# Kernel optimization log

Hardware: AMD Instinct MI355X
Metric: run time of the kernel (lower is better)

## Reference

```python
import jax, jax.numpy as jnp
import numpy as np

B, N, F_IN, K, NUM_CLASSES = 16, 2048, 8, 35, 4
EPS = 1e-5


def _bn(x, g, b):
    # BatchNorm in training mode: stats over all leading (batch/node/edge) dims.
    ax = tuple(range(x.ndim - 1))
    mu = jnp.mean(x, axis=ax, keepdims=True)
    var = jnp.var(x, axis=ax, keepdims=True)
    return g * (x - mu) * jax.lax.rsqrt(var + EPS) + b


def _edge_feats(h, k):
    # h: [B,N,C]. Dynamic kNN within each graph (self included, as torch_cluster.knn),
    # then EdgeConv features cat([x_i, x_j - x_i]) -> [B,N,k,2C].
    sq = jnp.sum(h * h, -1)                                   # [B,N]
    d = sq[:, :, None] + sq[:, None, :] - 2.0 * jnp.einsum('bnc,bmc->bnm', h, h)
    _, idx = jax.lax.top_k(-d, k)                             # [B,N,k]
    hj = jax.vmap(lambda hb, ib: hb[ib])(h, idx)              # [B,N,k,C]
    hi = jnp.broadcast_to(h[:, :, None, :], hj.shape)
    return jnp.concatenate([hi, hj - hi], axis=-1)


def _forward(x, w1, b1, g1, bt1, w2, b2, g2, bt2, w3, b3, w4, b4,
             w5, b5, w6, b6, g6, bt6, w7, b7, g7, bt7, w8, b8):
    # conv1: DynamicEdgeConv(MLP([16,64,64,64]), k, 'max'); plain_last => 3rd linear bare
    e = _edge_feats(x, K)                                     # [B,N,K,16]
    h = jax.nn.relu(_bn(e @ w1 + b1, g1, bt1))
    h = jax.nn.relu(_bn(h @ w2 + b2, g2, bt2))
    h = h @ w3 + b3
    x1 = jnp.max(h, axis=2)                                   # [B,N,64] scatter-max over k
    # conv2: DynamicEdgeConv(MLP([128,128]), k, 'max'); single plain linear
    e2 = _edge_feats(x1, K)                                   # [B,N,K,128]
    x2 = jnp.max(e2 @ w4 + b4, axis=2)                        # [B,N,128]
    out = jnp.concatenate([x1, x2], axis=-1) @ w5 + b5        # [B,N,256]
    pooled = jnp.max(out, axis=1)                             # [B,256] global_max_pool
    # head MLP([256,128,64,4], dropout eval-mode, batch_norm), plain_last
    h = jax.nn.relu(_bn(pooled @ w6 + b6, g6, bt6))
    h = jax.nn.relu(_bn(h @ w7 + b7, g7, bt7))
    return h @ w8 + b8                                        # [B,4]


def setup_inputs() -> dict:
    key = jax.random.key(0)
    ks = jax.random.split(key, 12)

    def lin(kk, fi, fo):
        k1, k2 = jax.random.split(kk)
        w = jax.random.normal(k1, (fi, fo), jnp.float32) / np.sqrt(fi).astype(np.float32)
        b = jax.random.normal(k2, (fo,), jnp.float32) * 0.01
        return w, b

    x = jax.random.normal(ks[0], (B, N, F_IN), jnp.float32)
    w1, b1 = lin(ks[1], 2 * F_IN, 64)
    w2, b2 = lin(ks[2], 64, 64)
    w3, b3 = lin(ks[3], 64, 64)
    w4, b4 = lin(ks[4], 2 * 64, 128)
    w5, b5 = lin(ks[5], 128 + 64, 256)
    w6, b6 = lin(ks[6], 256, 128)
    w7, b7 = lin(ks[7], 128, 64)
    w8, b8 = lin(ks[8], 64, NUM_CLASSES)
    ones, zeros = jnp.ones, jnp.zeros
    return {
        'x': x,
        'w1': w1, 'b1': b1, 'g1': ones(64), 'bt1': zeros(64),
        'w2': w2, 'b2': b2, 'g2': ones(64), 'bt2': zeros(64),
        'w3': w3, 'b3': b3,
        'w4': w4, 'b4': b4,
        'w5': w5, 'b5': b5,
        'w6': w6, 'b6': b6, 'g6': ones(128), 'bt6': zeros(128),
        'w7': w7, 'b7': b7, 'g7': ones(64), 'bt7': zeros(64),
        'w8': w8, 'b8': b8,
    }


def reference(x, w1, b1, g1, bt1, w2, b2, g2, bt2, w3, b3, w4, b4,
              w5, b5, w6, b6, g6, bt6, w7, b7, g7, bt7, w8, b8):
    return _forward(x, w1, b1, g1, bt1, w2, b2, g2, bt2, w3, b3, w4, b4,
                    w5, b5, w6, b6, g6, bt6, w7, b7, g7, bt7, w8, b8)
```

## Files before the change

kernel.cpp:

```cpp
#include <hip/hip_runtime.h>
#include <cfloat>
#include <cstdint>

constexpr int Bn   = 16;
constexpr int Nn   = 2048;
constexpr int Fin  = 8;
constexpr int Kn   = 35;
constexpr int NODES = Bn * Nn;
constexpr int EDG   = NODES * Kn;
constexpr int NSTATB = 1024;
constexpr float EPSV = 1e-5f;

typedef _Float16 f16;
typedef _Float16 f16x2 __attribute__((ext_vector_type(2)));

__device__ __forceinline__ unsigned enc_f(float f){
    unsigned u = __float_as_uint(f);
    return (u & 0x80000000u) ? ~u : (u | 0x80000000u);
}
__device__ __forceinline__ float dec_f(unsigned e){
    unsigned u = (e & 0x80000000u) ? (e ^ 0x80000000u) : ~e;
    return __uint_as_float(u);
}

template<int C>
__global__ __launch_bounds__(256) void sq_kernel(const float* __restrict__ h, float* __restrict__ sq){
    int i = blockIdx.x * 256 + threadIdx.x;
    if (i >= NODES) return;
    const float* p = h + (size_t)i * C;
    float s = 0.f;
#pragma unroll
    for (int c = 0; c < C; c++) s += p[c] * p[c];
    sq[i] = s;
}

template<int C>
__global__ __launch_bounds__(256) void knn_kernel(const float* __restrict__ h, const float* __restrict__ sq,
                                                  int* __restrict__ idxout){
    __shared__ float dist[4][Nn];
    __shared__ float hi4[4][C];
    __shared__ float sqi[4];
    __shared__ float statred[4][3][4];
    __shared__ __align__(16) unsigned long long keybuf[4][64];
    int t  = threadIdx.x;
    int b  = blockIdx.x >> 9;
    int i0 = (blockIdx.x & 511) * 4;
    int w  = t >> 6, lane = t & 63;

    for (int i = t; i < 4 * C; i += 256)
        hi4[i / C][i % C] = h[((size_t)(b * Nn) + i0 + i / C) * C + (i % C)];
    if (t < 4) sqi[t] = sq[b * Nn + i0 + t];
    __syncthreads();

    const float4* H0 = (const float4*)hi4[0];
    const float4* H1 = (const float4*)hi4[1];
    const float4* H2 = (const float4*)hi4[2];
    const float4* H3 = (const float4*)hi4[3];
    float ps0=0.f,ps1=0.f,ps2=0.f,ps3=0.f, pq0=0.f,pq1=0.f,pq2=0.f,pq3=0.f;
    float mn0=FLT_MAX,mn1=FLT_MAX,mn2=FLT_MAX,mn3=FLT_MAX;
    for (int j = t; j < Nn; j += 256){
        const float4* hj = (const float4*)(h + ((size_t)(b * Nn) + j) * C);
        float d0 = 0.f, d1 = 0.f, d2 = 0.f, d3 = 0.f;
#pragma unroll 4
        for (int c4 = 0; c4 < C / 4; c4++){
            float4 v = hj[c4];
            float4 a0 = H0[c4], a1 = H1[c4], a2 = H2[c4], a3 = H3[c4];
            d0 += a0.x*v.x + a0.y*v.y + a0.z*v.z + a0.w*v.w;
            d1 += a1.x*v.x + a1.y*v.y + a1.z*v.z + a1.w*v.w;
            d2 += a2.x*v.x + a2.y*v.y + a2.z*v.z + a2.w*v.w;
            d3 += a3.x*v.x + a3.y*v.y + a3.z*v.z + a3.w*v.w;
        }
        float sj = sq[b * Nn + j];
        float D0 = sqi[0] + sj - 2.f*d0; dist[0][j] = D0; ps0 += D0; pq0 += D0*D0; mn0 = fminf(mn0, D0);
        float D1 = sqi[1] + sj - 2.f*d1; dist[1][j] = D1; ps1 += D1; pq1 += D1*D1; mn1 = fminf(mn1, D1);
        float D2 = sqi[2] + sj - 2.f*d2; dist[2][j] = D2; ps2 += D2; pq2 += D2*D2; mn2 = fminf(mn2, D2);
        float D3 = sqi[3] + sj - 2.f*d3; dist[3][j] = D3; ps3 += D3; pq3 += D3*D3; mn3 = fminf(mn3, D3);
    }
#pragma unroll
    for (int d = 1; d < 64; d <<= 1){
        ps0 += __shfl_xor(ps0, d); pq0 += __shfl_xor(pq0, d); mn0 = fminf(mn0, __shfl_xor(mn0, d));
        ps1 += __shfl_xor(ps1, d); pq1 += __shfl_xor(pq1, d); mn1 = fminf(mn1, __shfl_xor(mn1, d));
        ps2 += __shfl_xor(ps2, d); pq2 += __shfl_xor(pq2, d); mn2 = fminf(mn2, __shfl_xor(mn2, d));
        ps3 += __shfl_xor(ps3, d); pq3 += __shfl_xor(pq3, d); mn3 = fminf(mn3, __shfl_xor(mn3, d));
    }
    if (lane == 0){
        statred[0][0][w] = ps0; statred[0][1][w] = pq0; statred[0][2][w] = mn0;
        statred[1][0][w] = ps1; statred[1][1][w] = pq1; statred[1][2][w] = mn1;
        statred[2][0][w] = ps2; statred[2][1][w] = pq2; statred[2][2][w] = mn2;
        statred[3][0][w] = ps3; statred[3][1][w] = pq3; statred[3][2][w] = mn3;
    }
    __syncthreads();

    const float* dw = dist[w];
    float smu = statred[w][0][0] + statred[w][0][1] + statred[w][0][2] + statred[w][0][3];
    float mnq = fminf(fminf(statred[w][2][0], statred[w][2][1]),
                      fminf(statred[w][2][2], statred[w][2][3]));
    float mu = smu * (1.f / (float)Nn);
    float span = fmaxf(mu - mnq, 0.f);

    float lo = mnq;  int clo = 0;
    float hi = FLT_MAX;  int chi = Nn;

    float PV[5] = { mnq + 0.25f*span, mnq + 0.40f*span, mnq + 0.55f*span,
                    mnq + 0.75f*span, mu };
    int c0 = 0, c1 = 0, c2 = 0, c3 = 0, c4 = 0;
    for (int s8 = 0; s8 < 32; s8 += 8){
        float vv[8];
#pragma unroll
        for (int u = 0; u < 8; u++) vv[u] = dw[(s8 + u) * 64 + lane];
#pragma unroll
        for (int u = 0; u < 8; u++){
            float v = vv[u];
            c0 += (v < PV[0]) ? 1 : 0;
            c1 += (v < PV[1]) ? 1 : 0;
            c2 += (v < PV[2]) ? 1 : 0;
            c3 += (v < PV[3]) ? 1 : 0;
            c4 += (v < PV[4]) ? 1 : 0;
        }
    }
#pragma unroll
    for (int d = 1; d < 64; d <<= 1){
        c0 += __shfl_xor(c0, d);
        c1 += __shfl_xor(c1, d);
        c2 += __shfl_xor(c2, d);
        c3 += __shfl_xor(c3, d);
        c4 += __shfl_xor(c4, d);
    }
    {
        int CC[5] = {c0, c1, c2, c3, c4};
#pragma unroll
        for (int pi = 0; pi < 5; pi++){
            if (CC[pi] >= Kn){ if (PV[pi] < hi){ hi = PV[pi]; chi = CC[pi]; } }
            else             { if (PV[pi] > lo){ lo = PV[pi]; clo = CC[pi]; } }
        }
    }

    for (int it = 0; it < 24 && chi > 64; it++){
        int den = (chi - clo) > 0 ? (chi - clo) : 1;
        float piv = (it & 1) ? 0.5f * (lo + hi)
                             : lo + (hi - lo) * ((float)(48 - clo) / (float)den);
        if (!(piv > lo && piv < hi)) piv = 0.5f * (lo + hi);
        if (!(piv > lo && piv < hi)) break;
        int c = 0;
        for (int s8 = 0; s8 < 32; s8 += 8){
            float vv[8];
#pragma unroll
            for (int u = 0; u < 8; u++) vv[u] = dw[(s8 + u) * 64 + lane];
#pragma unroll
            for (int u = 0; u < 8; u++) c += (vv[u] < piv) ? 1 : 0;
        }
#pragma unroll
        for (int d = 1; d < 64; d <<= 1) c += __shfl_xor(c, d);
        if (c >= Kn){ hi = piv; chi = c; } else { lo = piv; clo = c; }
    }

    size_t obase = ((size_t)(b * Nn) + i0 + w) * Kn;

    if (chi <= 64){
        keybuf[w][lane] = ~0ull;
        unsigned long long me_lower = (1ull << lane) - 1ull;
        int boff = 0;
        for (int s8 = 0; s8 < 32; s8 += 8){
            float vv[8];
#pragma unroll
            for (int u = 0; u < 8; u++) vv[u] = dw[(s8 + u) * 64 + lane];
#pragma unroll
            for (int u = 0; u < 8; u++){
                bool cnd = vv[u] < hi;
                unsigned long long m = __ballot(cnd);
                if (cnd){
                    int o = boff + __popcll(m & me_lower);
                    keybuf[w][o] = (((unsigned long long)enc_f(vv[u])) << 16) | (unsigned)((s8 + u) * 64 + lane);
                }
                boff += __popcll(m);
            }
        }
        unsigned long long k0 = keybuf[w][lane];
        int r0 = 0;
        int nR = (chi + 7) & ~7;
        const ulonglong2* kb2 = (const ulonglong2*)keybuf[w];
        for (int j2 = 0; j2 < nR; j2 += 8){
            ulonglong2 A = kb2[(j2 >> 1) + 0];
            ulonglong2 B = kb2[(j2 >> 1) + 1];
            ulonglong2 Cx = kb2[(j2 >> 1) + 2];
            ulonglong2 D = kb2[(j2 >> 1) + 3];
            r0 += (A.x<k0)+(A.y<k0)+(B.x<k0)+(B.y<k0)+(Cx.x<k0)+(Cx.y<k0)+(D.x<k0)+(D.y<k0);
        }
        if (lane < chi && r0 < Kn) idxout[obase + r0] = (int)(k0 & 0xffffu);
    } else {
        unsigned selmask = 0u;
        for (int e = 0; e < Kn; e++){
            unsigned long long best = ~0ull;
#pragma unroll
            for (int s = 0; s < 32; s++){
                float v = dw[s * 64 + lane];
                if (v < hi && !((selmask >> s) & 1)){
                    unsigned long long key = (((unsigned long long)enc_f(v)) << 16) | (unsigned)(s * 64 + lane);
                    best = (key < best) ? key : best;
                }
            }
#pragma unroll
            for (int d = 1; d < 64; d <<= 1){
                unsigned long long ov = __shfl_xor(best, d);
                best = (ov < best) ? ov : best;
            }
            int jj = (int)(best & 0xffffu);
            if ((jj & 63) == lane) selmask |= 1u << (jj >> 6);
            if (lane == 0) idxout[obase + e] = jj;
        }
    }
}

__global__ __launch_bounds__(256) void pre1_kernel(const float* __restrict__ x,
        const float* __restrict__ w1, const float* __restrict__ b1,
        float* __restrict__ p, float* __restrict__ q){
    int t = threadIdx.x, w = t >> 6, c = t & 63;
    float wd[8], wb[8];
#pragma unroll
    for (int f = 0; f < 8; f++){
        float wbv = w1[(8 + f) * 64 + c];
        wb[f] = wbv;
        wd[f] = w1[f * 64 + c] - wbv;
    }
    float b1c = b1[c];
    int slot = blockIdx.x * 4 + w;
    for (int it = 0; it < 16; it++){
        int node = slot + it * 2048;
        const float* xp = x + (size_t)node * Fin;
        float pv = b1c, qv = 0.f;
#pragma unroll
        for (int f = 0; f < 8; f++){
            float xv = xp[f];
            pv += xv * wd[f]; qv += xv * wb[f];
        }
        p[(size_t)node * 64 + c] = pv;
        q[(size_t)node * 64 + c] = qv;
    }
}

__global__ __launch_bounds__(256) void stats1_kernel(const float* __restrict__ p, const float* __restrict__ q,
        const int* __restrict__ idx, float* __restrict__ sumP, float* __restrict__ ssqP){
    __shared__ float red[2][4][64];
    int t = threadIdx.x, w = t >> 6, c = t & 63;
    float s = 0.f, ss = 0.f;
    int slot = blockIdx.x * 4 + w;
    for (int it = 0; it < 8; it++){
        int node = slot + it * 4096;
        int b = node >> 11;
        float pc = p[(size_t)node * 64 + c];
        const int* ip = idx + (size_t)node * Kn;
        for (int k = 0; k < Kn; k++){
            int j = ip[k];
            float z = pc + q[((size_t)(b << 11) + j) * 64 + c];
            s += z; ss += z * z;
        }
    }
    red[0][w][c] = s; red[1][w][c] = ss;
    __syncthreads();
    if (w == 0){
        sumP[blockIdx.x * 64 + c] = red[0][0][c] + red[0][1][c] + red[0][2][c] + red[0][3][c];
        ssqP[blockIdx.x * 64 + c] = red[1][0][c] + red[1][1][c] + red[1][2][c] + red[1][3][c];
    }
}

__global__ void finalize_kernel(const float* __restrict__ sumP, const float* __restrict__ ssqP,
        const float* __restrict__ gg, const float* __restrict__ bt,
        float* __restrict__ scale, float* __restrict__ shift, float inv_count){
    int c = threadIdx.x;
    float s = 0.f, q = 0.f;
    for (int i = 0; i < NSTATB; i++){ s += sumP[i * 64 + c]; q += ssqP[i * 64 + c]; }
    float mu  = s * inv_count;
    float var = q * inv_count - mu * mu;
    float sc  = gg[c] / sqrtf(var + EPSV);
    scale[c] = sc;
    shift[c] = bt[c] - mu * sc;
}

__global__ __launch_bounds__(256) void stats2_kernel(const float* __restrict__ p, const float* __restrict__ q,
        const int* __restrict__ idx,
        const float* __restrict__ sc1v, const float* __restrict__ sh1v,
        const float* __restrict__ w2, const float* __restrict__ b2,
        float* __restrict__ sumP, float* __restrict__ ssqP){
    __shared__ __align__(16) f16 hsh[4][2][64];
    __shared__ float red[2][4][64];
    int t = threadIdx.x, w = t >> 6, c = t & 63;
    f16x2 w2h[32];
#pragma unroll
    for (int f2 = 0; f2 < 32; f2++)
        w2h[f2] = f16x2{(f16)w2[(2*f2)*64 + c], (f16)w2[(2*f2+1)*64 + c]};
    float sc1 = sc1v[c], sh1 = sh1v[c], b2c = b2[c];
    float s = 0.f, ss = 0.f;
    int slot = blockIdx.x * 4 + w;
    for (int it = 0; it < 8; it++){
        int node = slot + it * 4096;
        int b = node >> 11;
        float pc = p[(size_t)node * 64 + c];
        const int* ip = idx + (size_t)node * Kn;
        for (int k = 0; k < Kn; k += 2){
            bool two = (k + 1 < Kn);
            int j0 = ip[k];
            int j1 = ip[two ? k + 1 : k];
            float za = pc + q[((size_t)(b << 11) + j0) * 64 + c];
            float zb = pc + q[((size_t)(b << 11) + j1) * 64 + c];
            hsh[w][0][c] = (f16)fmaxf(0.f, za * sc1 + sh1);
            hsh[w][1][c] = (f16)fmaxf(0.f, zb * sc1 + sh1);
            const uint4* h40 = (const uint4*)hsh[w][0];
            const uint4* h41 = (const uint4*)hsh[w][1];
            float p00=0.f,p01=0.f,p02=0.f,p03=0.f, p10=0.f,p11=0.f,p12=0.f,p13=0.f;
#pragma unroll
            for (int i = 0; i < 8; i++){
                uint4 u0 = h40[i], u1 = h41[i];
                p00 = __builtin_amdgcn_fdot2(__builtin_bit_cast(f16x2, u0.x), w2h[4*i+0], p00, false);
                p10 = __builtin_amdgcn_fdot2(__builtin_bit_cast(f16x2, u1.x), w2h[4*i+0], p10, false);
                p01 = __builtin_amdgcn_fdot2(__builtin_bit_cast(f16x2, u0.y), w2h[4*i+1], p01, false);
                p11 = __builtin_amdgcn_fdot2(__builtin_bit_cast(f16x2, u1.y), w2h[4*i+1], p11, false);
                p02 = __builtin_amdgcn_fdot2(__builtin_bit_cast(f16x2, u0.z), w2h[4*i+2], p02, false);
                p12 = __builtin_amdgcn_fdot2(__builtin_bit_cast(f16x2, u1.z), w2h[4*i+2], p12, false);
                p03 = __builtin_amdgcn_fdot2(__builtin_bit_cast(f16x2, u0.w), w2h[4*i+3], p03, false);
                p13 = __builtin_amdgcn_fdot2(__builtin_bit_cast(f16x2, u1.w), w2h[4*i+3], p13, false);
            }
            float z20 = b2c + ((p00 + p01) + (p02 + p03));
            float z21 = b2c + ((p10 + p11) + (p12 + p13));
            s += z20; ss += z20 * z20;
            if (two){ s += z21; ss += z21 * z21; }
        }
    }
    red[0][w][c] = s; red[1][w][c] = ss;
    __syncthreads();
    if (w == 0){
        sumP[blockIdx.x * 64 + c] = red[0][0][c] + red[0][1][c] + red[0][2][c] + red[0][3][c];
        ssqP[blockIdx.x * 64 + c] = red[1][0][c] + red[1][1][c] + red[1][2][c] + red[1][3][c];
    }
}

__global__ __launch_bounds__(256) void conv1_kernel(const float* __restrict__ p, const float* __restrict__ q,
        const int* __restrict__ idx,
        const float* __restrict__ sc1v, const float* __restrict__ sh1v,
        const float* __restrict__ w2, const float* __restrict__ b2,
        const float* __restrict__ sc2v, const float* __restrict__ sh2v,
        const float* __restrict__ w3, const float* __restrict__ b3,
        float* __restrict__ x1){
    __shared__ __align__(16) f16 hA[4][2][64];
    __shared__ __align__(16) f16 hB[4][2][64];
    int t = threadIdx.x, w = t >> 6, c = t & 63;
    f16x2 w2h[32], w3h[32];
#pragma unroll
    for (int f2 = 0; f2 < 32; f2++){
        w2h[f2] = f16x2{(f16)w2[(2*f2)*64 + c], (f16)w2[(2*f2+1)*64 + c]};
        w3h[f2] = f16x2{(f16)w3[(2*f2)*64 + c], (f16)w3[(2*f2+1)*64 + c]};
    }
    float sc1 = sc1v[c], sh1 = sh1v[c], sc2 = sc2v[c], sh2 = sh2v[c];
    float b2c = b2[c], b3c = b3[c];
    int node = blockIdx.x * 4 + w;
    int b = node >> 11;
    float pc = p[(size_t)node * 64 + c];
    const int* ip = idx + (size_t)node * Kn;
    float acc = -FLT_MAX;
    for (int k = 0; k < Kn; k += 2){
        bool two = (k + 1 < Kn);
        int j0 = ip[k];
        int j1 = ip[two ? k + 1 : k];
        float za = pc + q[((size_t)(b << 11) + j0) * 64 + c];
        float zb = pc + q[((size_t)(b << 11) + j1) * 64 + c];
        hA[w][0][c] = (f16)fmaxf(0.f, za * sc1 + sh1);
        hA[w][1][c] = (f16)fmaxf(0.f, zb * sc1 + sh1);
        const uint4* h40 = (const uint4*)hA[w][0];
        const uint4* h41 = (const uint4*)hA[w][1];
        float p00=0.f,p01=0.f,p02=0.f,p03=0.f, p10=0.f,p11=0.f,p12=0.f,p13=0.f;
#pragma unroll
        for (int i = 0; i < 8; i++){
            uint4 u0 = h40[i], u1 = h41[i];
            p00 = __builtin_amdgcn_fdot2(__builtin_bit_cast(f16x2, u0.x), w2h[4*i+0], p00, false);
            p10 = __builtin_amdgcn_fdot2(__builtin_bit_cast(f16x2, u1.x), w2h[4*i+0], p10, false);
            p01 = __builtin_amdgcn_fdot2(__builtin_bit_cast(f16x2, u0.y), w2h[4*i+1], p01, false);
            p11 = __builtin_amdgcn_fdot2(__builtin_bit_cast(f16x2, u1.y), w2h[4*i+1], p11, false);
            p02 = __builtin_amdgcn_fdot2(__builtin_bit_cast(f16x2, u0.z), w2h[4*i+2], p02, false);
            p12 = __builtin_amdgcn_fdot2(__builtin_bit_cast(f16x2, u1.z), w2h[4*i+2], p12, false);
            p03 = __builtin_amdgcn_fdot2(__builtin_bit_cast(f16x2, u0.w), w2h[4*i+3], p03, false);
            p13 = __builtin_amdgcn_fdot2(__builtin_bit_cast(f16x2, u1.w), w2h[4*i+3], p13, false);
        }
        float z20 = b2c + ((p00 + p01) + (p02 + p03));
        float z21 = b2c + ((p10 + p11) + (p12 + p13));
        hB[w][0][c] = (f16)fmaxf(0.f, z20 * sc2 + sh2);
        hB[w][1][c] = (f16)fmaxf(0.f, z21 * sc2 + sh2);
        const uint4* g40 = (const uint4*)hB[w][0];
        const uint4* g41 = (const uint4*)hB[w][1];
        float q00=0.f,q01=0.f,q02=0.f,q03=0.f, q10=0.f,q11=0.f,q12=0.f,q13=0.f;
#pragma unroll
        for (int i = 0; i < 8; i++){
            uint4 u0 = g40[i], u1 = g41[i];
            q00 = __builtin_amdgcn_fdot2(__builtin_bit_cast(f16x2, u0.x), w3h[4*i+0], q00, false);
            q10 = __builtin_amdgcn_fdot2(__builtin_bit_cast(f16x2, u1.x), w3h[4*i+0], q10, false);
            q01 = __builtin_amdgcn_fdot2(__builtin_bit_cast(f16x2, u0.y), w3h[4*i+1], q01, false);
            q11 = __builtin_amdgcn_fdot2(__builtin_bit_cast(f16x2, u1.y), w3h[4*i+1], q11, false);
            q02 = __builtin_amdgcn_fdot2(__builtin_bit_cast(f16x2, u0.z), w3h[4*i+2], q02, false);
            q12 = __builtin_amdgcn_fdot2(__builtin_bit_cast(f16x2, u1.z), w3h[4*i+2], q12, false);
            q03 = __builtin_amdgcn_fdot2(__builtin_bit_cast(f16x2, u0.w), w3h[4*i+3], q03, false);
            q13 = __builtin_amdgcn_fdot2(__builtin_bit_cast(f16x2, u1.w), w3h[4*i+3], q13, false);
        }
        float z30 = b3c + ((q00 + q01) + (q02 + q03));
        float z31 = b3c + ((q10 + q11) + (q12 + q13));
        acc = fmaxf(acc, z30);
        if (two) acc = fmaxf(acc, z31);
    }
    x1[(size_t)node * 64 + c] = acc;
}

__global__ __launch_bounds__(256) void pre2_kernel(const float* __restrict__ x1,
        const float* __restrict__ w4, const float* __restrict__ b4,
        float* __restrict__ u, float* __restrict__ v){
    __shared__ float x1s[16][64];
    int t = threadIdx.x;
    int c = t & 127, h = t >> 7;
    float wd[64], wb[64];
#pragma unroll
    for (int f = 0; f < 64; f++){
        float wbv = w4[(64 + f) * 128 + c];
        wb[f] = wbv;
        wd[f] = w4[f * 128 + c] - wbv;
    }
    float b4c = b4[c];
    int base = blockIdx.x * 16;
    for (int i = t; i < 16 * 64; i += 256)
        x1s[i >> 6][i & 63] = x1[(size_t)(base + (i >> 6)) * 64 + (i & 63)];
    __syncthreads();
    for (int n = 0; n < 8; n++){
        int node = base + h * 8 + n;
        const float4* xr = (const float4*)x1s[h * 8 + n];
        float u0 = 0.f, u1 = 0.f, v0 = 0.f, v1 = 0.f;
#pragma unroll
        for (int f4 = 0; f4 < 16; f4++){
            float4 xv = xr[f4];
            float pa = xv.x * wd[4*f4] + xv.y * wd[4*f4+1] + xv.z * wd[4*f4+2] + xv.w * wd[4*f4+3];
            float pb = xv.x * wb[4*f4] + xv.y * wb[4*f4+1] + xv.z * wb[4*f4+2] + xv.w * wb[4*f4+3];
            if (f4 & 1){ u1 += pa; v1 += pb; } else { u0 += pa; v0 += pb; }
        }
        u[(size_t)node * 128 + c] = b4c + u0 + u1;
        v[(size_t)node * 128 + c] = v0 + v1;
    }
}

__global__ __launch_bounds__(256) void gmax2_kernel(const float* __restrict__ v, const int* __restrict__ idx,
        float* __restrict__ x2){
    int t = threadIdx.x, g = t >> 7, c = t & 127;
    int node = blockIdx.x * 2 + g;
    int b = node >> 11;
    const int* ip = idx + (size_t)node * Kn;
    float vm = -FLT_MAX;
    for (int k = 0; k < Kn; k++){
        int j = ip[k];
        vm = fmaxf(vm, v[((size_t)(b << 11) + j) * 128 + c]);
    }
    x2[(size_t)node * 128 + c] += vm;
}

__global__ __launch_bounds__(256) void outpool_kernel(const float* __restrict__ x1, const float* __restrict__ x2,
        const float* __restrict__ w5, const float* __restrict__ b5, unsigned* __restrict__ pooled){
    __shared__ float rows[8][192];
    int t = threadIdx.x;
    int node0 = blockIdx.x * 8;
    for (int i = t; i < 8 * 192; i += 256){
        int e = i / 192, f = i - e * 192;
        int nd = node0 + e;
        rows[e][f] = (f < 64) ? x1[(size_t)nd * 64 + f] : x2[(size_t)nd * 128 + f - 64];
    }
    __syncthreads();
    float z[8];
#pragma unroll
    for (int e = 0; e < 8; e++) z[e] = b5[t];
    for (int f = 0; f < 192; f++){
        float w = w5[f * 256 + t];
#pragma unroll
        for (int e = 0; e < 8; e++) z[e] += rows[e][f] * w;
    }
    float m = z[0];
#pragma unroll
    for (int e = 1; e < 8; e++) m = fmaxf(m, z[e]);
    int b = node0 >> 11;
    atomicMax(&pooled[b * 256 + t], enc_f(m));
}

__global__ __launch_bounds__(256) void head_kernel(const unsigned* __restrict__ pooledE,
        const float* __restrict__ w6, const float* __restrict__ b6, const float* __restrict__ g6, const float* __restrict__ bt6,
        const float* __restrict__ w7, const float* __restrict__ b7, const float* __restrict__ g7, const float* __restrict__ bt7,
        const float* __restrict__ w8, const float* __restrict__ b8, float* __restrict__ out){
    __shared__ float P[16][256];
    __shared__ float H6[16][128];
    __shared__ float H7[16][64];
    int t = threadIdx.x;
    for (int i = t; i < 16 * 256; i += 256) P[i >> 8][i & 255] = dec_f(pooledE[i]);
    __syncthreads();
    for (int i = t; i < 16 * 128; i += 256){
        int r = i >> 7, c = i & 127;
        float z = b6[c];
        for (int f = 0; f < 256; f++) z += P[r][f] * w6[f * 128 + c];
        H6[r][c] = z;
    }
    __syncthreads();
    if (t < 128){
        float s = 0.f, q = 0.f;
        for (int r = 0; r < 16; r++){ float v = H6[r][t]; s += v; q += v * v; }
        float mu = s * (1.f / 16.f);
        float var = q * (1.f / 16.f) - mu * mu;
        float sc = g6[t] / sqrtf(var + EPSV);
        float sh = bt6[t] - mu * sc;
        for (int r = 0; r < 16; r++) H6[r][t] = fmaxf(0.f, H6[r][t] * sc + sh);
    }
    __syncthreads();
    for (int i = t; i < 16 * 64; i += 256){
        int r = i >> 6, c = i & 63;
        float z = b7[c];
        for (int f = 0; f < 128; f++) z += H6[r][f] * w7[f * 64 + c];
        H7[r][c] = z;
    }
    __syncthreads();
    if (t < 64){
        float s = 0.f, q = 0.f;
        for (int r = 0; r < 16; r++){ float v = H7[r][t]; s += v; q += v * v; }
        float mu = s * (1.f / 16.f);
        float var = q * (1.f / 16.f) - mu * mu;
        float sc = g7[t] / sqrtf(var + EPSV);
        float sh = bt7[t] - mu * sc;
        for (int r = 0; r < 16; r++) H7[r][t] = fmaxf(0.f, H7[r][t] * sc + sh);
    }
    __syncthreads();
    if (t < 64){
        int r = t >> 2, c = t & 3;
        float z = b8[c];
        for (int f = 0; f < 64; f++) z += H7[r][f] * w8[f * 4 + c];
        out[t] = z;
    }
}

extern "C" void kernel_launch(void* const* d_in, const int* in_sizes, int n_in,
                              void* d_out, int out_size, void* d_ws, size_t ws_size,
                              hipStream_t stream){
    const float* x   = (const float*)d_in[0];
    const float* w1  = (const float*)d_in[1];
    const float* b1  = (const float*)d_in[2];
    const float* g1  = (const float*)d_in[3];
    const float* bt1 = (const float*)d_in[4];
    const float* w2  = (const float*)d_in[5];
    const float* b2  = (const float*)d_in[6];
    const float* g2  = (const float*)d_in[7];
    const float* bt2 = (const float*)d_in[8];
    const float* w3  = (const float*)d_in[9];
    const float* b3  = (const float*)d_in[10];
    const float* w4  = (const float*)d_in[11];
    const float* b4  = (const float*)d_in[12];
    const float* w5  = (const float*)d_in[13];
    const float* b5  = (const float*)d_in[14];
    const float* w6  = (const float*)d_in[15];
    const float* b6  = (const float*)d_in[16];
    const float* g6  = (const float*)d_in[17];
    const float* bt6 = (const float*)d_in[18];
    const float* w7  = (const float*)d_in[19];
    const float* b7  = (const float*)d_in[20];
    const float* g7  = (const float*)d_in[21];
    const float* bt7 = (const float*)d_in[22];
    const float* w8  = (const float*)d_in[23];
    const float* b8  = (const float*)d_in[24];
    float* out = (float*)d_out;

    char* ws = (char*)d_ws;
    size_t off = 0;
    auto alloc = [&](size_t bytes)->char*{
        char* p = ws + off;
        off += (bytes + 255) & ~(size_t)255;
        return p;
    };
    int*      idx1   = (int*)alloc((size_t)EDG * 4);
    int*      idx2   = (int*)alloc((size_t)EDG * 4);
    float*    sq1    = (float*)alloc((size_t)NODES * 4);
    float*    sq2    = (float*)alloc((size_t)NODES * 4);
    float*    x1     = (float*)alloc((size_t)NODES * 64 * 4);
    float*    x2     = (float*)alloc((size_t)NODES * 128 * 4);
    float*    sumP   = (float*)alloc((size_t)NSTATB * 64 * 4);
    float*    ssqP   = (float*)alloc((size_t)NSTATB * 64 * 4);
    float*    scale1 = (float*)alloc(64 * 4);
    float*    shift1 = (float*)alloc(64 * 4);
    float*    scale2 = (float*)alloc(64 * 4);
    float*    shift2 = (float*)alloc(64 * 4);
    unsigned* pooled = (unsigned*)alloc((size_t)Bn * 256 * 4);
    float*    p      = (float*)alloc((size_t)NODES * 64 * 4);
    float*    q      = (float*)alloc((size_t)NODES * 64 * 4);
    float*    v      = p;

    hipMemsetAsync(pooled, 0, (size_t)Bn * 256 * 4, stream);

    sq_kernel<8><<<(NODES + 255) / 256, 256, 0, stream>>>(x, sq1);
    knn_kernel<8><<<NODES / 4, 256, 0, stream>>>(x, sq1, idx1);
    pre1_kernel<<<512, 256, 0, stream>>>(x, w1, b1, p, q);
    stats1_kernel<<<NSTATB, 256, 0, stream>>>(p, q, idx1, sumP, ssqP);
    finalize_kernel<<<1, 64, 0, stream>>>(sumP, ssqP, g1, bt1, scale1, shift1, 1.0f / (float)EDG);
    stats2_kernel<<<NSTATB, 256, 0, stream>>>(p, q, idx1, scale1, shift1, w2, b2, sumP, ssqP);
    finalize_kernel<<<1, 64, 0, stream>>>(sumP, ssqP, g2, bt2, scale2, shift2, 1.0f / (float)EDG);
    conv1_kernel<<<NODES / 4, 256, 0, stream>>>(p, q, idx1, scale1, shift1,
                                                w2, b2, scale2, shift2, w3, b3, x1);
    sq_kernel<64><<<(NODES + 255) / 256, 256, 0, stream>>>(x1, sq2);
    knn_kernel<64><<<NODES / 4, 256, 0, stream>>>(x1, sq2, idx2);
    pre2_kernel<<<NODES / 16, 256, 0, stream>>>(x1, w4, b4, x2, v);
    gmax2_kernel<<<NODES / 2, 256, 0, stream>>>(v, idx2, x2);
    outpool_kernel<<<NODES / 8, 256, 0, stream>>>(x1, x2, w5, b5, pooled);
    head_kernel<<<1, 256, 0, stream>>>(pooled, w6, b6, g6, bt6, w7, b7, g7, bt7, w8, b8, out);
}
```

Baseline: 1.321 ms.

## Keep kNN distances in registers and select cooperatively across the whole block

Drops the 32KB shared-memory distance array. Each thread now holds its 8 distances for all 4 query rows in registers. Pivot counting, refinement and candidate compaction become block-wide: per-wave partial counts are reduced through small shared arrays, and candidates are appended to per-query buffers with shared atomics. The goal is to cut LDS traffic and raise occupancy, at the cost of more registers, extra __syncthreads per iteration, fewer refinement iterations, and a slower block-wide fallback selection that uses barriers.

```diff
diff --git a/kernel.cpp b/kernel.cpp
--- a/kernel.cpp
+++ b/kernel.cpp
@@ -37,11 +37,14 @@
 template<int C>
 __global__ __launch_bounds__(256) void knn_kernel(const float* __restrict__ h, const float* __restrict__ sq,
                                                   int* __restrict__ idxout){
-    __shared__ float dist[4][Nn];
     __shared__ float hi4[4][C];
     __shared__ float sqi[4];
-    __shared__ float statred[4][3][4];
+    __shared__ float statred[3][4][4];
+    __shared__ int   cntred[4][4][4];
+    __shared__ int   cnt1[4][4];
+    __shared__ int   cslot[4];
     __shared__ __align__(16) unsigned long long keybuf[4][64];
+    __shared__ unsigned long long fbred[4];
     int t  = threadIdx.x;
     int b  = blockIdx.x >> 9;
     int i0 = (blockIdx.x & 511) * 4;
@@ -51,14 +54,19 @@
         hi4[i / C][i % C] = h[((size_t)(b * Nn) + i0 + i / C) * C + (i % C)];
     if (t < 4) sqi[t] = sq[b * Nn + i0 + t];
     __syncthreads();
+    float sqq0 = sqi[0], sqq1 = sqi[1], sqq2 = sqi[2], sqq3 = sqi[3];
 
     const float4* H0 = (const float4*)hi4[0];
     const float4* H1 = (const float4*)hi4[1];
     const float4* H2 = (const float4*)hi4[2];
     const float4* H3 = (const float4*)hi4[3];
-    float ps0=0.f,ps1=0.f,ps2=0.f,ps3=0.f, pq0=0.f,pq1=0.f,pq2=0.f,pq3=0.f;
-    float mn0=FLT_MAX,mn1=FLT_MAX,mn2=FLT_MAX,mn3=FLT_MAX;
-    for (int j = t; j < Nn; j += 256){
+
+    float D[4][8];
+    float ps[4] = {0.f,0.f,0.f,0.f}, pq[4] = {0.f,0.f,0.f,0.f};
+    float mn[4] = {FLT_MAX,FLT_MAX,FLT_MAX,FLT_MAX};
+#pragma unroll
+    for (int jj = 0; jj < 8; jj++){
+        int j = t + jj * 256;
         const float4* hj = (const float4*)(h + ((size_t)(b * Nn) + j) * C);
         float d0 = 0.f, d1 = 0.f, d2 = 0.f, d3 = 0.f;
 #pragma unroll 4
@@ -71,142 +79,200 @@
             d3 += a3.x*v.x + a3.y*v.y + a3.z*v.z + a3.w*v.w;
         }
         float sj = sq[b * Nn + j];
-        float D0 = sqi[0] + sj - 2.f*d0; dist[0][j] = D0; ps0 += D0; pq0 += D0*D0; mn0 = fminf(mn0, D0);
-        float D1 = sqi[1] + sj - 2.f*d1; dist[1][j] = D1; ps1 += D1; pq1 += D1*D1; mn1 = fminf(mn1, D1);
-        float D2 = sqi[2] + sj - 2.f*d2; dist[2][j] = D2; ps2 += D2; pq2 += D2*D2; mn2 = fminf(mn2, D2);
-        float D3 = sqi[3] + sj - 2.f*d3; dist[3][j] = D3; ps3 += D3; pq3 += D3*D3; mn3 = fminf(mn3, D3);
+        float v0 = sqq0 + sj - 2.f*d0; D[0][jj] = v0; ps[0] += v0; pq[0] += v0*v0; mn[0] = fminf(mn[0], v0);
+        float v1 = sqq1 + sj - 2.f*d1; D[1][jj] = v1; ps[1] += v1; pq[1] += v1*v1; mn[1] = fminf(mn[1], v1);
+        float v2 = sqq2 + sj - 2.f*d2; D[2][jj] = v2; ps[2] += v2; pq[2] += v2*v2; mn[2] = fminf(mn[2], v2);
+        float v3 = sqq3 + sj - 2.f*d3; D[3][jj] = v3; ps[3] += v3; pq[3] += v3*v3; mn[3] = fminf(mn[3], v3);
     }
 #pragma unroll
     for (int d = 1; d < 64; d <<= 1){
-        ps0 += __shfl_xor(ps0, d); pq0 += __shfl_xor(pq0, d); mn0 = fminf(mn0, __shfl_xor(mn0, d));
-        ps1 += __shfl_xor(ps1, d); pq1 += __shfl_xor(pq1, d); mn1 = fminf(mn1, __shfl_xor(mn1, d));
-        ps2 += __shfl_xor(ps2, d); pq2 += __shfl_xor(pq2, d); mn2 = fminf(mn2, __shfl_xor(mn2, d));
-        ps3 += __shfl_xor(ps3, d); pq3 += __shfl_xor(pq3, d); mn3 = fminf(mn3, __shfl_xor(mn3, d));
+#pragma unroll
+        for (int q = 0; q < 4; q++){
+            ps[q] += __shfl_xor(ps[q], d);
+            pq[q] += __shfl_xor(pq[q], d);
+            mn[q] = fminf(mn[q], __shfl_xor(mn[q], d));
+        }
     }
     if (lane == 0){
-        statred[0][0][w] = ps0; statred[0][1][w] = pq0; statred[0][2][w] = mn0;
-        statred[1][0][w] = ps1; statred[1][1][w] = pq1; statred[1][2][w] = mn1;
-        statred[2][0][w] = ps2; statred[2][1][w] = pq2; statred[2][2][w] = mn2;
-        statred[3][0][w] = ps3; statred[3][1][w] = pq3; statred[3][2][w] = mn3;
-    }
-    __syncthreads();
-
-    const float* dw = dist[w];
-    float smu = statred[w][0][0] + statred[w][0][1] + statred[w][0][2] + statred[w][0][3];
-    float mnq = fminf(fminf(statred[w][2][0], statred[w][2][1]),
-                      fminf(statred[w][2][2], statred[w][2][3]));
-    float mu = smu * (1.f / (float)Nn);
-    float span = fmaxf(mu - mnq, 0.f);
-
-    float lo = mnq;  int clo = 0;
-    float hi = FLT_MAX;  int chi = Nn;
-
-    float PV[5] = { mnq + 0.25f*span, mnq + 0.40f*span, mnq + 0.55f*span,
-                    mnq + 0.75f*span, mu };
-    int c0 = 0, c1 = 0, c2 = 0, c3 = 0, c4 = 0;
-    for (int s8 = 0; s8 < 32; s8 += 8){
-        float vv[8];
-#pragma unroll
-        for (int u = 0; u < 8; u++) vv[u] = dw[(s8 + u) * 64 + lane];
-#pragma unroll
-        for (int u = 0; u < 8; u++){
-            float v = vv[u];
-            c0 += (v < PV[0]) ? 1 : 0;
-            c1 += (v < PV[1]) ? 1 : 0;
-            c2 += (v < PV[2]) ? 1 : 0;
-            c3 += (v < PV[3]) ? 1 : 0;
-            c4 += (v < PV[4]) ? 1 : 0;
-        }
-    }
-#pragma unroll
-    for (int d = 1; d < 64; d <<= 1){
-        c0 += __shfl_xor(c0, d);
-        c1 += __shfl_xor(c1, d);
-        c2 += __shfl_xor(c2, d);
-        c3 += __shfl_xor(c3, d);
-        c4 += __shfl_xor(c4, d);
-    }
+#pragma unroll
+        for (int q = 0; q < 4; q++){
+            statred[0][q][w] = ps[q]; statred[1][q][w] = pq[q]; statred[2][q][w] = mn[q];
+        }
+    }
+    __syncthreads();
+
+    float muq[4], mnq[4], loq[4], hiq[4];
+    int cloq[4], chiq[4];
+    float PVq[4][4];
+#pragma unroll
+    for (int q = 0; q < 4; q++){
+        float s = statred[0][q][0] + statred[0][q][1] + statred[0][q][2] + statred[0][q][3];
+        float m = fminf(fminf(statred[2][q][0], statred[2][q][1]),
+                        fminf(statred[2][q][2], statred[2][q][3]));
+        muq[q] = s * (1.f / (float)Nn); mnq[q] = m;
+        float span = fmaxf(muq[q] - m, 0.f);
+        PVq[q][0] = m + 0.25f*span; PVq[q][1] = m + 0.42f*span;
+        PVq[q][2] = m + 0.62f*span; PVq[q][3] = muq[q];
+        loq[q] = m; cloq[q] = 0; hiq[q] = FLT_MAX; chiq[q] = Nn;
+    }
+
     {
-        int CC[5] = {c0, c1, c2, c3, c4};
-#pragma unroll
-        for (int pi = 0; pi < 5; pi++){
-            if (CC[pi] >= Kn){ if (PV[pi] < hi){ hi = PV[pi]; chi = CC[pi]; } }
-            else             { if (PV[pi] > lo){ lo = PV[pi]; clo = CC[pi]; } }
-        }
-    }
-
-    for (int it = 0; it < 24 && chi > 64; it++){
-        int den = (chi - clo) > 0 ? (chi - clo) : 1;
-        float piv = (it & 1) ? 0.5f * (lo + hi)
-                             : lo + (hi - lo) * ((float)(48 - clo) / (float)den);
-        if (!(piv > lo && piv < hi)) piv = 0.5f * (lo + hi);
-        if (!(piv > lo && piv < hi)) break;
-        int c = 0;
-        for (int s8 = 0; s8 < 32; s8 += 8){
-            float vv[8];
-#pragma unroll
-            for (int u = 0; u < 8; u++) vv[u] = dw[(s8 + u) * 64 + lane];
-#pragma unroll
-            for (int u = 0; u < 8; u++) c += (vv[u] < piv) ? 1 : 0;
-        }
-#pragma unroll
-        for (int d = 1; d < 64; d <<= 1) c += __shfl_xor(c, d);
-        if (c >= Kn){ hi = piv; chi = c; } else { lo = piv; clo = c; }
-    }
+        int lc[4][4];
+#pragma unroll
+        for (int q = 0; q < 4; q++)
+#pragma unroll
+        for (int pi = 0; pi < 4; pi++){
+            int acc = 0;
+#pragma unroll
+            for (int jj = 0; jj < 8; jj++) acc += (D[q][jj] < PVq[q][pi]) ? 1 : 0;
+            lc[q][pi] = acc;
+        }
+#pragma unroll
+        for (int d = 1; d < 64; d <<= 1){
+#pragma unroll
+            for (int q = 0; q < 4; q++)
+#pragma unroll
+            for (int pi = 0; pi < 4; pi++) lc[q][pi] += __shfl_xor(lc[q][pi], d);
+        }
+        if (lane == 0){
+#pragma unroll
+            for (int q = 0; q < 4; q++)
+#pragma unroll
+            for (int pi = 0; pi < 4; pi++) cntred[pi][q][w] = lc[q][pi];
+        }
+    }
+    __syncthreads();
+#pragma unroll
+    for (int q = 0; q < 4; q++){
+#pragma unroll
+        for (int pi = 0; pi < 4; pi++){
+            int CCv = cntred[pi][q][0] + cntred[pi][q][1] + cntred[pi][q][2] + cntred[pi][q][3];
+            if (CCv >= Kn){ if (PVq[q][pi] < hiq[q]){ hiq[q] = PVq[q][pi]; chiq[q] = CCv; } }
+            else          { if (PVq[q][pi] > loq[q]){ loq[q] = PVq[q][pi]; cloq[q] = CCv; } }
+        }
+    }
+
+    for (int it = 0; it < 12; it++){
+        bool any = false;
+        float piv[4]; bool act[4];
+#pragma unroll
+        for (int q = 0; q < 4; q++){
+            act[q] = (chiq[q] > 64);
+            piv[q] = 0.f;
+            if (act[q]){
+                int den = (chiq[q] - cloq[q]) > 0 ? (chiq[q] - cloq[q]) : 1;
+                float pv = (it & 1) ? 0.5f * (loq[q] + hiq[q])
+                                    : loq[q] + (hiq[q] - loq[q]) * ((float)(48 - cloq[q]) / (float)den);
+                if (!(pv > loq[q] && pv < hiq[q])) pv = 0.5f * (loq[q] + hiq[q]);
+                if (!(pv > loq[q] && pv < hiq[q])) act[q] = false;
+                piv[q] = pv;
+            }
+            any = any || act[q];
+        }
+        if (!any) break;
+        int lc1[4] = {0,0,0,0};
+#pragma unroll
+        for (int q = 0; q < 4; q++){
+            if (act[q]){
+                int acc = 0;
+#pragma unroll
+                for (int jj = 0; jj < 8; jj++) acc += (D[q][jj] < piv[q]) ? 1 : 0;
+                lc1[q] = acc;
+            }
+        }
+#pragma unroll
+        for (int d = 1; d < 64; d <<= 1){
+#pragma unroll
+            for (int q = 0; q < 4; q++) lc1[q] += __shfl_xor(lc1[q], d);
+        }
+        if (lane == 0){
+#pragma unroll
+            for (int q = 0; q < 4; q++) cnt1[q][w] = lc1[q];
+        }
+        __syncthreads();
+#pragma unroll
+        for (int q = 0; q < 4; q++){
+            if (act[q]){
+                int ct = cnt1[q][0] + cnt1[q][1] + cnt1[q][2] + cnt1[q][3];
+                if (ct >= Kn){ if (piv[q] < hiq[q]){ hiq[q] = piv[q]; chiq[q] = ct; } }
+                else         { if (piv[q] > loq[q]){ loq[q] = piv[q]; cloq[q] = ct; } }
+            }
+        }
+        __syncthreads();
+    }
+
+    keybuf[w][lane] = ~0ull;
+    if (t < 4) cslot[t] = 0;
+    __syncthreads();
+#pragma unroll
+    for (int q = 0; q < 4; q++){
+        if (chiq[q] <= 64){
+#pragma unroll
+            for (int jj = 0; jj < 8; jj++){
+                float v = D[q][jj];
+                if (v < hiq[q]){
+                    int o = atomicAdd(&cslot[q], 1);
+                    if (o < 64)
+                        keybuf[q][o] = (((unsigned long long)enc_f(v)) << 16) | (unsigned)(t + jj * 256);
+                }
+            }
+        }
+    }
+    __syncthreads();
 
     size_t obase = ((size_t)(b * Nn) + i0 + w) * Kn;
-
-    if (chi <= 64){
-        keybuf[w][lane] = ~0ull;
-        unsigned long long me_lower = (1ull << lane) - 1ull;
-        int boff = 0;
-        for (int s8 = 0; s8 < 32; s8 += 8){
-            float vv[8];
-#pragma unroll
-            for (int u = 0; u < 8; u++) vv[u] = dw[(s8 + u) * 64 + lane];
-#pragma unroll
-            for (int u = 0; u < 8; u++){
-                bool cnd = vv[u] < hi;
-                unsigned long long m = __ballot(cnd);
-                if (cnd){
-                    int o = boff + __popcll(m & me_lower);
-                    keybuf[w][o] = (((unsigned long long)enc_f(vv[u])) << 16) | (unsigned)((s8 + u) * 64 + lane);
-                }
-                boff += __popcll(m);
-            }
-        }
+    int chiw = (w == 0) ? chiq[0] : (w == 1) ? chiq[1] : (w == 2) ? chiq[2] : chiq[3];
+    if (chiw <= 64){
         unsigned long long k0 = keybuf[w][lane];
         int r0 = 0;
-        int nR = (chi + 7) & ~7;
+        int nR = (chiw + 7) & ~7;
         const ulonglong2* kb2 = (const ulonglong2*)keybuf[w];
         for (int j2 = 0; j2 < nR; j2 += 8){
             ulonglong2 A = kb2[(j2 >> 1) + 0];
             ulonglong2 B = kb2[(j2 >> 1) + 1];
             ulonglong2 Cx = kb2[(j2 >> 1) + 2];
-            ulonglong2 D = kb2[(j2 >> 1) + 3];
-            r0 += (A.x<k0)+(A.y<k0)+(B.x<k0)+(B.y<k0)+(Cx.x<k0)+(Cx.y<k0)+(D.x<k0)+(D.y<k0);
-        }
-        if (lane < chi && r0 < Kn) idxout[obase + r0] = (int)(k0 & 0xffffu);
-    } else {
-        unsigned selmask = 0u;
-        for (int e = 0; e < Kn; e++){
-            unsigned long long best = ~0ull;
-#pragma unroll
-            for (int s = 0; s < 32; s++){
-                float v = dw[s * 64 + lane];
-                if (v < hi && !((selmask >> s) & 1)){
-                    unsigned long long key = (((unsigned long long)enc_f(v)) << 16) | (unsigned)(s * 64 + lane);
-                    best = (key < best) ? key : best;
+            ulonglong2 Dd = kb2[(j2 >> 1) + 3];
+            r0 += (A.x<k0)+(A.y<k0)+(B.x<k0)+(B.y<k0)+(Cx.x<k0)+(Cx.y<k0)+(Dd.x<k0)+(Dd.y<k0);
+        }
+        if (lane < chiw && r0 < Kn) idxout[obase + r0] = (int)(k0 & 0xffffu);
+    }
+
+#pragma unroll
+    for (int q = 0; q < 4; q++){
+        if (chiq[q] > 64){
+            size_t ob = ((size_t)(b * Nn) + i0 + q) * Kn;
+            unsigned selm = 0;
+            for (int e = 0; e < Kn; e++){
+                unsigned long long best = ~0ull;
+#pragma unroll
+                for (int jj = 0; jj < 8; jj++){
+                    float v = D[q][jj];
+                    if (v < hiq[q] && !((selm >> jj) & 1)){
+                        unsigned long long key = (((unsigned long long)enc_f(v)) << 16) | (unsigned)(t + jj * 256);
+                        best = (key < best) ? key : best;
+                    }
                 }
+#pragma unroll
+                for (int d = 1; d < 64; d <<= 1){
+                    unsigned long long ov = __shfl_xor(best, d);
+                    best = (ov < best) ? ov : best;
+                }
+                if (lane == 0) fbred[w] = best;
+                __syncthreads();
+                unsigned long long g = fbred[0];
+                g = (fbred[1] < g) ? fbred[1] : g;
+                g = (fbred[2] < g) ? fbred[2] : g;
+                g = (fbred[3] < g) ? fbred[3] : g;
+#pragma unroll
+                for (int jj = 0; jj < 8; jj++){
+                    float v = D[q][jj];
+                    if (v < hiq[q]){
+                        unsigned long long key = (((unsigned long long)enc_f(v)) << 16) | (unsigned)(t + jj * 256);
+                        if (key == g){ selm |= 1u << jj; idxout[ob + e] = (int)(g & 0xffffu); }
+                    }
+                }
+                __syncthreads();
             }
-#pragma unroll
-            for (int d = 1; d < 64; d <<= 1){
-                unsigned long long ov = __shfl_xor(best, d);
-                best = (ov < best) ? ov : best;
-            }
-            int jj = (int)(best & 0xffffu);
-            if ((jj & 63) == lane) selmask |= 1u << (jj >> 6);
-            if (lane == 0) idxout[obase + e] = jj;
         }
     }
 }
```

Result: slower. 1.400 ms (+6.0%).
